# Kernel optimization log

Measured on AMD Instinct MI355X. Metric: run time of the kernel, lower is better.

The kernel has to match this reference:

```python
import jax, jax.numpy as jnp
import numpy as np

DIM, HEADS = 128, 8
DH = DIM // HEADS
SCALE = DH ** -0.5
N, E = 50000, 800000


def setup_inputs() -> dict:
    key = jax.random.key(0)
    ks = jax.random.split(key, 12)
    w = lambda k: jax.random.normal(k, (DIM, DIM), dtype=jnp.float32) * 0.02
    b = lambda k: jax.random.normal(k, (DIM,), dtype=jnp.float32) * 0.02
    return {
        "q_nodes": jax.random.normal(ks[0], (N, DIM), dtype=jnp.float32),
        "k_edges": jax.random.normal(ks[1], (E, DIM), dtype=jnp.float32),
        "v_edges": jax.random.normal(ks[2], (E, DIM), dtype=jnp.float32),
        "edge_index": jax.random.randint(ks[3], (2, E), 0, N, dtype=jnp.int64),
        "Wq": w(ks[4]), "bq": b(ks[5]),
        "Wk": w(ks[6]), "bk": b(ks[7]),
        "Wv": w(ks[8]), "bv": b(ks[9]),
        "Wo": w(ks[10]), "bo": b(ks[11]),
    }


def reference(q_nodes, k_edges, v_edges, edge_index, Wq, bq, Wk, bk, Wv, bv, Wo, bo):
    n, e = q_nodes.shape[0], k_edges.shape[0]
    dst = edge_index[0]  # src (edge_index[1]) is unused by the module
    q = (q_nodes @ Wq.T + bq).reshape(n, HEADS, DH)
    k = (k_edges @ Wk.T + bk).reshape(e, HEADS, DH)
    v = (v_edges @ Wv.T + bv).reshape(e, HEADS, DH)
    # per-edge score: dot(q[dst], k) per head -> [E, H]
    score = jnp.einsum('ehd,ehd->eh', q[dst], k) * SCALE
    # segment (per-dst-node) softmax over edges, numerically stable
    m = jax.ops.segment_max(score, dst, num_segments=n)          # [N, H]
    ex = jnp.exp(score - m[dst])                                  # [E, H]
    s = jax.ops.segment_sum(ex, dst, num_segments=n)             # [N, H]
    w = ex / (s[dst] + 1e-16)                                     # [E, H]
    weighted_v = (v * w[..., None]).reshape(e, DIM)               # [E, dim]
    aggr = jax.ops.segment_sum(weighted_v, dst, num_segments=n)  # [N, dim]
    return aggr @ Wo.T + bo
```

## Files before the change

kernel.cpp:

```cpp
#include <hip/hip_runtime.h>

#define TM 64
#define NTHREADS 256
#define PAD 132

typedef __attribute__((ext_vector_type(8))) short short8;
typedef __attribute__((ext_vector_type(4))) float f32x4;

__device__ __forceinline__ short f2bf(float f) {
  union { float f; unsigned u; } uf; uf.f = f;
  unsigned r = uf.u + 0x7FFFu + ((uf.u >> 16) & 1u);
  return (short)(r >> 16);
}
__device__ __forceinline__ float bf2f(short s) {
  union { unsigned u; float f; } uf; uf.u = ((unsigned)(unsigned short)s) << 16;
  return uf.f;
}
__device__ __forceinline__ short8 pack8(float4 a, float4 b) {
  short8 r;
  r[0] = f2bf(a.x); r[1] = f2bf(a.y); r[2] = f2bf(a.z); r[3] = f2bf(a.w);
  r[4] = f2bf(b.x); r[5] = f2bf(b.y); r[6] = f2bf(b.z); r[7] = f2bf(b.w);
  return r;
}


__global__ __launch_bounds__(512) void proj_mfma(
    const float* __restrict__ X, const short* __restrict__ Wb,
    const float* __restrict__ bias, float* __restrict__ Y, int M, float scale) {
  __shared__ short Xb[8192];
  int t = threadIdx.x;
  int w = t >> 6, l = t & 63, g = l >> 4, c = l & 15;
  short8 wf[4];
#pragma unroll
  for (int kc = 0; kc < 4; ++kc)
    wf[kc] = *(const short8*)(Wb + (w * 16 + c) * 128 + kc * 32 + g * 8);
  float4 b4 = *(const float4*)(bias + w * 16 + g * 4);

  for (int rb = blockIdx.x * 64; rb < M; rb += gridDim.x * 64) {
    {
      int r = t >> 3, q8 = t & 7;
      int row = rb + r; if (row >= M) row = M - 1;
      const float4* xs = (const float4*)(X + (size_t)row * 128 + q8 * 16);
      float4 x0 = xs[0], x1 = xs[1], x2 = xs[2], x3 = xs[3];
      int sw = (r & 7) << 4;
      *(short8*)((char*)Xb + r * 256 + ((q8 * 32) ^ sw)) = pack8(x0, x1);
      *(short8*)((char*)Xb + r * 256 + ((q8 * 32 + 16) ^ sw)) = pack8(x2, x3);
    }
    __syncthreads();
#pragma unroll
    for (int et = 0; et < 4; ++et) {
      int rl = et * 16 + c;
      f32x4 acc = {};
      int sw = (rl & 7) << 4;
#pragma unroll
      for (int kc = 0; kc < 4; ++kc) {
        short8 xb = *(const short8*)((char*)Xb + rl * 256 + ((kc * 64 + g * 16) ^ sw));
        acc = __builtin_amdgcn_mfma_f32_16x16x32_bf16(wf[kc], xb, acc, 0, 0, 0);
      }
      int row = rb + rl;
      if (row < M) {
        float4 o;
        o.x = (acc[0] + b4.x) * scale; o.y = (acc[1] + b4.y) * scale;
        o.z = (acc[2] + b4.z) * scale; o.w = (acc[3] + b4.w) * scale;
        *(float4*)(Y + (size_t)row * 128 + w * 16 + g * 4) = o;
      }
    }
    __syncthreads();
  }
}


__global__ __launch_bounds__(512) void proj_mfma_h(
    const float* __restrict__ X, const short* __restrict__ Wb,
    const float* __restrict__ bias, short* __restrict__ Yh, int M, float scale) {
  __shared__ short Xb[8192];
  int t = threadIdx.x;
  int w = t >> 6, l = t & 63, g = l >> 4, c = l & 15;
  short8 wf[4];
#pragma unroll
  for (int kc = 0; kc < 4; ++kc)
    wf[kc] = *(const short8*)(Wb + (w * 16 + c) * 128 + kc * 32 + g * 8);
  float4 b4 = *(const float4*)(bias + w * 16 + g * 4);

  for (int rb = blockIdx.x * 64; rb < M; rb += gridDim.x * 64) {
    {
      int r = t >> 3, q8 = t & 7;
      int row = rb + r; if (row >= M) row = M - 1;
      const float4* xs = (const float4*)(X + (size_t)row * 128 + q8 * 16);
      float4 x0 = xs[0], x1 = xs[1], x2 = xs[2], x3 = xs[3];
      int sw = (r & 7) << 4;
      *(short8*)((char*)Xb + r * 256 + ((q8 * 32) ^ sw)) = pack8(x0, x1);
      *(short8*)((char*)Xb + r * 256 + ((q8 * 32 + 16) ^ sw)) = pack8(x2, x3);
    }
    __syncthreads();
#pragma unroll
    for (int et = 0; et < 4; ++et) {
      int rl = et * 16 + c;
      f32x4 acc = {};
      int sw = (rl & 7) << 4;
#pragma unroll
      for (int kc = 0; kc < 4; ++kc) {
        short8 xb = *(const short8*)((char*)Xb + rl * 256 + ((kc * 64 + g * 16) ^ sw));
        acc = __builtin_amdgcn_mfma_f32_16x16x32_bf16(wf[kc], xb, acc, 0, 0, 0);
      }
      int row = rb + rl;
      if (row < M) {
        short4 o;
        o.x = f2bf((acc[0] + b4.x) * scale); o.y = f2bf((acc[1] + b4.y) * scale);
        o.z = f2bf((acc[2] + b4.z) * scale); o.w = f2bf((acc[3] + b4.w) * scale);
        *(short4*)(Yh + (size_t)row * 128 + w * 16 + g * 4) = o;
      }
    }
    __syncthreads();
  }
}


__global__ __launch_bounds__(256) void hist_kernel(const int* __restrict__ dst,
                                                   int* __restrict__ cnt, int E) {
  int e = blockIdx.x * 256 + threadIdx.x;
  if (e < E) atomicAdd(&cnt[dst[e]], 1);
}

__global__ __launch_bounds__(1024) void scan_part(const int* __restrict__ cnt,
                                                  int* __restrict__ part, int N) {
  __shared__ int ws[16];
  int t = threadIdx.x, i = blockIdx.x * 1024 + t;
  int v = (i < N) ? cnt[i] : 0;
#pragma unroll
  for (int d = 1; d < 64; d <<= 1) v += __shfl_xor(v, d);
  if ((t & 63) == 0) ws[t >> 6] = v;
  __syncthreads();
  if (t < 16) {
    int x = ws[t];
#pragma unroll
    for (int d = 1; d < 16; d <<= 1) x += __shfl_xor(x, d);
    if (t == 0) part[blockIdx.x] = x;
  }
}

__global__ __launch_bounds__(64) void scan_offs(int* __restrict__ part, int P) {
  int t = threadIdx.x;
  int carry = 0;
  for (int base = 0; base < P; base += 64) {
    int i = base + t;
    int v = (i < P) ? part[i] : 0;
    int x = v;
#pragma unroll
    for (int d = 1; d < 64; d <<= 1) { int y = __shfl_up(x, d); if (t >= d) x += y; }
    if (i < P) part[i] = x - v + carry;
    carry += __shfl(x, 63);
  }
}

__global__ __launch_bounds__(1024) void scan_final(const int* __restrict__ cnt,
                                                   const int* __restrict__ part,
                                                   int* __restrict__ rp,
                                                   int* __restrict__ cur, int N) {
  __shared__ int ws[16];
  __shared__ int wofs[16];
  int t = threadIdx.x, i = blockIdx.x * 1024 + t;
  int lane = t & 63, wid = t >> 6;
  int v = (i < N) ? cnt[i] : 0;
  int x = v;
#pragma unroll
  for (int d = 1; d < 64; d <<= 1) { int y = __shfl_up(x, d); if (lane >= d) x += y; }
  if (lane == 63) ws[wid] = x;
  __syncthreads();
  if (t == 0) {
    int s = 0;
#pragma unroll
    for (int k2 = 0; k2 < 16; ++k2) { int tmp = ws[k2]; wofs[k2] = s; s += tmp; }
  }
  __syncthreads();
  int incl = x + wofs[wid] + part[blockIdx.x];
  int excl = incl - v;
  if (i < N) {
    rp[i] = excl; cur[i] = excl;
    if (i == N - 1) rp[N] = incl;
  }
}

__global__ __launch_bounds__(256) void perm_kernel(const int* __restrict__ dst,
                                                   int* __restrict__ cursor,
                                                   int* __restrict__ perm, int E) {
  int e = blockIdx.x * 256 + threadIdx.x;
  if (e < E) perm[e] = atomicAdd(&cursor[dst[e]], 1);
}

__global__ __launch_bounds__(256) void wprep4(
    const float* __restrict__ Wq, const float* __restrict__ Wk,
    const float* __restrict__ Wv, const float* __restrict__ Wo,
    short* __restrict__ wqb, short* __restrict__ wkb,
    short* __restrict__ wvb, short* __restrict__ wob) {
  int i = blockIdx.x * 256 + threadIdx.x;
  if (i < 16384) {
    wqb[i] = f2bf(Wq[i]); wkb[i] = f2bf(Wk[i]);
    wvb[i] = f2bf(Wv[i]); wob[i] = f2bf(Wo[i]);
  }
}


__global__ __launch_bounds__(512) void edge_mfma7(
    const float* __restrict__ K, const float* __restrict__ V,
    const int* __restrict__ eidx, const int* __restrict__ perm,
    const short* __restrict__ wkb, const short* __restrict__ wvb,
    const float* __restrict__ bk, const short* __restrict__ qpb,
    float* __restrict__ exb, short* __restrict__ wv, int E) {
  __shared__ short Kb[8192];
  __shared__ short Vb[8192];
  __shared__ float exs[512];
  __shared__ int sh_perm[64];
  int t = threadIdx.x;
  int w = t >> 6, l = t & 63, g = l >> 4, c = l & 15;
  float4 bk4 = *(const float4*)(bk + w * 16 + g * 4);
  const short* wkp = wkb + (w * 16 + c) * 128 + g * 8;
  const short* wvp = wvb + (w * 16 + c) * 128 + g * 8;
  const short* qpp = qpb + (size_t)(w * 16 + g * 4);

  int r = t >> 3, q8 = t & 7;
  int sw_st = (r & 7) << 4;
  int b0 = r * 256 + ((q8 * 32) ^ sw_st);
  int stride = gridDim.x * 64;
  int eb = blockIdx.x * 64;

  float4 k0, k1, k2, k3;
  short4 qvb[4];
  int prm_r;
  {
    int row0 = eb + r; if (row0 >= E) row0 = E - 1;
    const float4* ks = (const float4*)(K + (size_t)row0 * 128 + q8 * 16);
    k0 = ks[0]; k1 = ks[1]; k2 = ks[2]; k3 = ks[3];
    prm_r = perm[row0];
#pragma unroll
    for (int et = 0; et < 4; ++et) {
      int e = eb + et * 16 + c; if (e >= E) e = E - 1;
      qvb[et] = *(const short4*)(qpp + (size_t)eidx[e] * 128);
    }
  }

  for (; eb < E; eb += stride) {
    int ebn = eb + stride;
    bool hn = ebn < E;

    __syncthreads();
    *(short8*)((char*)Kb + b0) = pack8(k0, k1);
    *(short8*)((char*)Kb + (b0 ^ 16)) = pack8(k2, k3);
    if (q8 == 0) sh_perm[r] = prm_r;
    short8 wK[4];
#pragma unroll
    for (int kc = 0; kc < 4; ++kc)
      wK[kc] = *(const short8*)(wkp + kc * 32);
    float4 v0, v1, v2, v3;
    {
      int rowv = eb + r; if (rowv >= E) rowv = E - 1;
      const float4* vs = (const float4*)(V + (size_t)rowv * 128 + q8 * 16);
      v0 = vs[0]; v1 = vs[1]; v2 = vs[2]; v3 = vs[3];
    }
    __syncthreads();

    float ex[4];
#pragma unroll
    for (int et = 0; et < 4; ++et) {
      int eloc = et * 16 + c;
      int swr = (eloc & 7) << 4;
      f32x4 acc = {};
#pragma unroll
      for (int kc = 0; kc < 4; ++kc) {
        short8 xb = *(const short8*)((char*)Kb + eloc * 256 + ((kc * 64 + g * 16) ^ swr));
        acc = __builtin_amdgcn_mfma_f32_16x16x32_bf16(wK[kc], xb, acc, 0, 0, 0);
      }
      float s = (acc[0] + bk4.x) * bf2f(qvb[et].x) + (acc[1] + bk4.y) * bf2f(qvb[et].y) +
                (acc[2] + bk4.z) * bf2f(qvb[et].z) + (acc[3] + bk4.w) * bf2f(qvb[et].w);
      s += __shfl_xor(s, 16);
      s += __shfl_xor(s, 32);
      ex[et] = __expf(s);
      if (g == 0) exs[eloc * 8 + w] = ex[et];
    }

    *(short8*)((char*)Vb + b0) = pack8(v0, v1);
    *(short8*)((char*)Vb + (b0 ^ 16)) = pack8(v2, v3);
    short8 wV[4];
#pragma unroll
    for (int kc = 0; kc < 4; ++kc)
      wV[kc] = *(const short8*)(wvp + kc * 32);
    int prm_rn = 0;
    if (hn) {
      int rowk = ebn + r; if (rowk >= E) rowk = E - 1;
      const float4* ks = (const float4*)(K + (size_t)rowk * 128 + q8 * 16);
      k0 = ks[0]; k1 = ks[1]; k2 = ks[2]; k3 = ks[3];
      prm_rn = perm[rowk];
#pragma unroll
      for (int et = 0; et < 4; ++et) {
        int e = ebn + et * 16 + c; if (e >= E) e = E - 1;
        qvb[et] = *(const short4*)(qpp + (size_t)eidx[e] * 128);
      }
    }
    __syncthreads();

#pragma unroll
    for (int et = 0; et < 4; ++et) {
      int eloc = et * 16 + c;
      int swr = (eloc & 7) << 4;
      f32x4 acc = {};
#pragma unroll
      for (int kc = 0; kc < 4; ++kc) {
        short8 xb = *(const short8*)((char*)Vb + eloc * 256 + ((kc * 64 + g * 16) ^ swr));
        acc = __builtin_amdgcn_mfma_f32_16x16x32_bf16(wV[kc], xb, acc, 0, 0, 0);
      }
      short4 sv;
      sv.x = f2bf(acc[0] * ex[et]); sv.y = f2bf(acc[1] * ex[et]);
      sv.z = f2bf(acc[2] * ex[et]); sv.w = f2bf(acc[3] * ex[et]);
      *(short4*)((char*)Kb + eloc * 256 + ((w * 32 + g * 8) ^ swr)) = sv;
    }
    prm_r = prm_rn;
    __syncthreads();

    {
      int row = eb + r;
      if (row < E) {
        int slot = sh_perm[r];
        short8 a = *(const short8*)((char*)Kb + r * 256 + ((q8 * 32) ^ sw_st));
        short8 b = *(const short8*)((char*)Kb + r * 256 + ((q8 * 32 + 16) ^ sw_st));
        *(short8*)(wv + (size_t)slot * 128 + q8 * 16) = a;
        *(short8*)(wv + (size_t)slot * 128 + q8 * 16 + 8) = b;
      }
      if (t < 128) {
        int r2 = t >> 1, half = t & 1;
        if (eb + r2 < E) {
          int slot2 = sh_perm[r2];
          *(float4*)(exb + (size_t)slot2 * 8 + half * 4) =
              *(const float4*)(&exs[r2 * 8 + half * 4]);
        }
      }
    }
  }
}


__global__ __launch_bounds__(256) void pull3(
    const short* __restrict__ wv, const float* __restrict__ exb,
    const int* __restrict__ rp, const float* __restrict__ bv,
    float* __restrict__ aggr, int N) {
  int w = threadIdx.x >> 6, l = threadIdx.x & 63;
  int n = blockIdx.x * 4 + w;
  if (n >= N) return;
  int beg = rp[n], end = rp[n + 1];
  int h = l >> 3;
  float a0 = 0.f, a1 = 0.f, s = 0.f;
  int j = beg;
  for (; j + 1 < end; j += 2) {
    unsigned u0 = *(const unsigned*)(wv + (size_t)j * 128 + l * 2);
    unsigned u1 = *(const unsigned*)(wv + (size_t)(j + 1) * 128 + l * 2);
    float s0 = exb[(size_t)j * 8 + h], s1 = exb[(size_t)(j + 1) * 8 + h];
    a0 += bf2f((short)(u0 & 0xFFFFu)) + bf2f((short)(u1 & 0xFFFFu));
    a1 += bf2f((short)(u0 >> 16)) + bf2f((short)(u1 >> 16));
    s += s0 + s1;
  }
  if (j < end) {
    unsigned u0 = *(const unsigned*)(wv + (size_t)j * 128 + l * 2);
    s += exb[(size_t)j * 8 + h];
    a0 += bf2f((short)(u0 & 0xFFFFu));
    a1 += bf2f((short)(u0 >> 16));
  }
  float2 o;
  if (end > beg) {
    float inv = 1.f / (s + 1e-16f);
    float2 bvv = *(const float2*)(bv + l * 2);
    o.x = a0 * inv + bvv.x; o.y = a1 * inv + bvv.y;
  } else {
    o.x = 0.f; o.y = 0.f;
  }
  *(float2*)(aggr + (size_t)n * 128 + l * 2) = o;
}


__device__ __forceinline__ void stage_x(float (*Xs)[PAD], const float* __restrict__ X,
                                        int rowbase, int M, int t) {
#pragma unroll
  for (int i = 0; i < 8; ++i) {
    int idx = t + NTHREADS * i;
    int r = idx >> 5, q = idx & 31;
    int row = rowbase + r;
    if (row >= M) row = M - 1;
    const float4 v = *(const float4*)(X + (size_t)row * 128 + q * 4);
    *(float4*)(&Xs[r][q * 4]) = v;
  }
}

__device__ __forceinline__ void gemm_tile(const float (*Xs)[PAD], float (*WT)[PAD],
                                          const float* __restrict__ W,
                                          float acc[8][4], int r0, int c0, int t) {
#pragma unroll 1
  for (int kk = 0; kk < 128; kk += 32) {
    {
      int j = t >> 1, half = t & 1;
      const float* src = W + j * 128 + kk + half * 16;
      float4 a = *(const float4*)(src);
      float4 b = *(const float4*)(src + 4);
      float4 c = *(const float4*)(src + 8);
      float4 d = *(const float4*)(src + 12);
      int cb = half * 16;
      WT[cb + 0][j] = a.x;  WT[cb + 1][j] = a.y;  WT[cb + 2][j] = a.z;  WT[cb + 3][j] = a.w;
      WT[cb + 4][j] = b.x;  WT[cb + 5][j] = b.y;  WT[cb + 6][j] = b.z;  WT[cb + 7][j] = b.w;
      WT[cb + 8][j] = c.x;  WT[cb + 9][j] = c.y;  WT[cb + 10][j] = c.z; WT[cb + 11][j] = c.w;
      WT[cb + 12][j] = d.x; WT[cb + 13][j] = d.y; WT[cb + 14][j] = d.z; WT[cb + 15][j] = d.w;
    }
    __syncthreads();
#pragma unroll
    for (int c2 = 0; c2 < 16; ++c2) {
      float4 wa = *(const float4*)(&WT[2 * c2][c0]);
      float4 wb = *(const float4*)(&WT[2 * c2 + 1][c0]);
#pragma unroll
      for (int i = 0; i < 8; ++i) {
        float2 xv = *(const float2*)(&Xs[r0 + i][kk + 2 * c2]);
        acc[i][0] = fmaf(xv.x, wa.x, acc[i][0]);
        acc[i][1] = fmaf(xv.x, wa.y, acc[i][1]);
        acc[i][2] = fmaf(xv.x, wa.z, acc[i][2]);
        acc[i][3] = fmaf(xv.x, wa.w, acc[i][3]);
        acc[i][0] = fmaf(xv.y, wb.x, acc[i][0]);
        acc[i][1] = fmaf(xv.y, wb.y, acc[i][1]);
        acc[i][2] = fmaf(xv.y, wb.z, acc[i][2]);
        acc[i][3] = fmaf(xv.y, wb.w, acc[i][3]);
      }
    }
    __syncthreads();
  }
}

__global__ __launch_bounds__(NTHREADS) void proj_kernel(
    const float* __restrict__ X, const float* __restrict__ W,
    const float* __restrict__ b, float* __restrict__ Y, int M) {
  __shared__ float Xs[TM][PAD];
  __shared__ float WT[32][PAD];
  int t = threadIdx.x;
  int B0 = blockIdx.x * TM;
  stage_x(Xs, X, B0, M, t);
  __syncthreads();
  int r0 = (t >> 5) * 8, m = t & 31, c0 = m * 4;
  float acc[8][4] = {};
  gemm_tile(Xs, WT, W, acc, r0, c0, t);
  float4 bv = ((const float4*)b)[m];
#pragma unroll
  for (int i = 0; i < 8; ++i) {
    int row = B0 + r0 + i;
    if (row < M) {
      float4 o;
      o.x = acc[i][0] + bv.x; o.y = acc[i][1] + bv.y;
      o.z = acc[i][2] + bv.z; o.w = acc[i][3] + bv.w;
      *(float4*)(Y + (size_t)row * 128 + c0) = o;
    }
  }
}

__global__ __launch_bounds__(NTHREADS) void edge_kernel(
    const float* __restrict__ Kin, const float* __restrict__ Vin,
    const int* __restrict__ eidx,
    const float* __restrict__ Wk, const float* __restrict__ bk,
    const float* __restrict__ Wv, const float* __restrict__ bv,
    const float* __restrict__ qp, float* __restrict__ s_sum,
    float* __restrict__ aggr, int E) {
  __shared__ float Xs[TM][PAD];
  __shared__ float WT[32][PAD];
  __shared__ int dsts[TM];
  int t = threadIdx.x;
  int e0 = blockIdx.x * TM;
  if (t < TM) {
    int idx = e0 + t;
    if (idx >= E) idx = E - 1;
    dsts[t] = eidx[idx];
  }
  stage_x(Xs, Kin, e0, E, t);
  __syncthreads();
  int r0 = (t >> 5) * 8, m = t & 31, c0 = m * 4;
  int h = m >> 2;
  float acc[8][4] = {};
  gemm_tile(Xs, WT, Wk, acc, r0, c0, t);
  float4 bkv = ((const float4*)bk)[m];
  float ex[8];
#pragma unroll
  for (int i = 0; i < 8; ++i) {
    int r = r0 + i;
    const float4 qv = *(const float4*)(qp + (size_t)dsts[r] * 128 + c0);
    float p = (acc[i][0] + bkv.x) * qv.x + (acc[i][1] + bkv.y) * qv.y +
              (acc[i][2] + bkv.z) * qv.z + (acc[i][3] + bkv.w) * qv.w;
    p += __shfl_xor(p, 1);
    p += __shfl_xor(p, 2);
    float e = __expf(p * 0.25f);
    ex[i] = e;
    if ((m & 3) == 0 && (e0 + r) < E)
      atomicAdd(&s_sum[(size_t)dsts[r] * 8 + h], e);
  }
  __syncthreads();
  stage_x(Xs, Vin, e0, E, t);
  __syncthreads();
#pragma unroll
  for (int i = 0; i < 8; ++i)
#pragma unroll
    for (int j = 0; j < 4; ++j) acc[i][j] = 0.f;
  gemm_tile(Xs, WT, Wv, acc, r0, c0, t);
  float4 bvv = ((const float4*)bv)[m];
#pragma unroll
  for (int i = 0; i < 8; ++i) {
    int r = r0 + i;
    if ((e0 + r) < E) {
      size_t base = (size_t)dsts[r] * 128 + c0;
      atomicAdd(&aggr[base + 0], (acc[i][0] + bvv.x) * ex[i]);
      atomicAdd(&aggr[base + 1], (acc[i][1] + bvv.y) * ex[i]);
      atomicAdd(&aggr[base + 2], (acc[i][2] + bvv.z) * ex[i]);
      atomicAdd(&aggr[base + 3], (acc[i][3] + bvv.w) * ex[i]);
    }
  }
}

__global__ __launch_bounds__(NTHREADS) void out_kernel(
    const float* __restrict__ aggr, const float* __restrict__ s_sum,
    const float* __restrict__ W, const float* __restrict__ b,
    float* __restrict__ Y, int M) {
  __shared__ float Xs[TM][PAD];
  __shared__ float WT[32][PAD];
  int t = threadIdx.x;
  int B0 = blockIdx.x * TM;
#pragma unroll
  for (int i = 0; i < 8; ++i) {
    int idx = t + NTHREADS * i;
    int r = idx >> 5, q = idx & 31;
    int row = B0 + r;
    if (row >= M) row = M - 1;
    float4 v = *(const float4*)(aggr + (size_t)row * 128 + q * 4);
    float inv = 1.0f / (s_sum[(size_t)row * 8 + (q >> 2)] + 1e-16f);
    v.x *= inv; v.y *= inv; v.z *= inv; v.w *= inv;
    *(float4*)(&Xs[r][q * 4]) = v;
  }
  __syncthreads();
  int r0 = (t >> 5) * 8, m = t & 31, c0 = m * 4;
  float acc[8][4] = {};
  gemm_tile(Xs, WT, W, acc, r0, c0, t);
  float4 bv = ((const float4*)b)[m];
#pragma unroll
  for (int i = 0; i < 8; ++i) {
    int row = B0 + r0 + i;
    if (row < M) {
      float4 o;
      o.x = acc[i][0] + bv.x; o.y = acc[i][1] + bv.y;
      o.z = acc[i][2] + bv.z; o.w = acc[i][3] + bv.w;
      *(float4*)(Y + (size_t)row * 128 + c0) = o;
    }
  }
}


extern "C" void kernel_launch(void* const* d_in, const int* in_sizes, int n_in,
                              void* d_out, int out_size, void* d_ws, size_t ws_size,
                              hipStream_t stream) {
  const float* q_nodes = (const float*)d_in[0];
  const float* k_edges = (const float*)d_in[1];
  const float* v_edges = (const float*)d_in[2];
  const int* eidx = (const int*)d_in[3];
  const float* Wq = (const float*)d_in[4];
  const float* bq = (const float*)d_in[5];
  const float* Wk = (const float*)d_in[6];
  const float* bk = (const float*)d_in[7];
  const float* Wv = (const float*)d_in[8];
  const float* bv = (const float*)d_in[9];
  const float* Wo = (const float*)d_in[10];
  const float* bo = (const float*)d_in[11];

  int N = in_sizes[0] / 128;
  int E = in_sizes[1] / 128;
  int P = (N + 1023) / 1024;

  size_t off = 0;
  auto alloc = [&](size_t b) { size_t o = off; off += (b + 255) & ~(size_t)255; return o; };
  size_t o_qpb  = alloc((size_t)N * 128 * 2);
  size_t o_aggr = alloc((size_t)N * 128 * 4);
  size_t o_exb  = alloc((size_t)E * 8 * 4);
  size_t o_rp   = alloc(((size_t)N + 1) * 4);
  size_t o_cur  = alloc((size_t)N * 4);
  size_t o_cnt  = alloc((size_t)N * 4);
  size_t o_perm = alloc((size_t)E * 4);
  size_t o_part = alloc((size_t)(P + 1) * 4);
  size_t o_wqb  = alloc((size_t)16384 * 2);
  size_t o_wkb  = alloc((size_t)16384 * 2);
  size_t o_wvb  = alloc((size_t)16384 * 2);
  size_t o_wob  = alloc((size_t)16384 * 2);
  size_t o_wv   = alloc((size_t)E * 128 * 2);

  if (off <= ws_size) {
    char* base = (char*)d_ws;
    short* qpb   = (short*)(base + o_qpb);
    float* aggr  = (float*)(base + o_aggr);
    float* exb   = (float*)(base + o_exb);
    int*   rp    = (int*)(base + o_rp);
    int*   cur   = (int*)(base + o_cur);
    int*   cnt   = (int*)(base + o_cnt);
    int*   perm  = (int*)(base + o_perm);
    int*   part  = (int*)(base + o_part);
    short* wqb   = (short*)(base + o_wqb);
    short* wkb   = (short*)(base + o_wkb);
    short* wvb   = (short*)(base + o_wvb);
    short* wob   = (short*)(base + o_wob);
    short* wvbuf = (short*)(base + o_wv);

    hipMemsetAsync(cnt, 0, (size_t)N * 4, stream);
    wprep4<<<64, 256, 0, stream>>>(Wq, Wk, Wv, Wo, wqb, wkb, wvb, wob);
    proj_mfma_h<<<(N + 63) / 64, 512, 0, stream>>>(q_nodes, wqb, bq, qpb, N, 0.25f);
    hist_kernel<<<(E + 255) / 256, 256, 0, stream>>>(eidx, cnt, E);
    scan_part<<<P, 1024, 0, stream>>>(cnt, part, N);
    scan_offs<<<1, 64, 0, stream>>>(part, P);
    scan_final<<<P, 1024, 0, stream>>>(cnt, part, rp, cur, N);
    perm_kernel<<<(E + 255) / 256, 256, 0, stream>>>(eidx, cur, perm, E);

    int eblk = (E + 63) / 64; if (eblk > 1024) eblk = 1024;
    edge_mfma7<<<eblk, 512, 0, stream>>>(k_edges, v_edges, eidx, perm, wkb, wvb,
                                         bk, qpb, exb, wvbuf, E);
    pull3<<<(N + 3) / 4, 256, 0, stream>>>(wvbuf, exb, rp, bv, aggr, N);
    proj_mfma<<<(N + 63) / 64, 512, 0, stream>>>(aggr, wob, bo, (float*)d_out, N, 1.0f);
  } else {
    float* q_proj = (float*)d_ws;
    float* s_sum  = q_proj + (size_t)N * 128;
    float* aggr   = s_sum + (size_t)N * 8;
    hipMemsetAsync(s_sum, 0, (size_t)N * 136 * sizeof(float), stream);
    int nblk = (N + TM - 1) / TM;
    int eblk = (E + TM - 1) / TM;
    proj_kernel<<<nblk, NTHREADS, 0, stream>>>(q_nodes, Wq, bq, q_proj, N);
    edge_kernel<<<eblk, NTHREADS, 0, stream>>>(k_edges, v_edges, eidx, Wk, bk, Wv, bv,
                                               q_proj, s_sum, aggr, E);
    out_kernel<<<nblk, NTHREADS, 0, stream>>>(aggr, s_sum, Wo, bo, (float*)d_out, N);
  }
}
```

Measured before the change: 420.0 us.

## Fuse histogram with rank capture and drop separate perm and offset-scan kernels

The histogram kernel now records each edge's atomic rank within its destination bucket, so the edge kernel computes its CSR slot as rp[dst]+rank and the second atomic pass (perm_kernel) disappears. The single-block offset scan is also removed: each scan_final block sums the preceding partials itself. This cuts two kernel launches and one full pass of atomics over the edges, at the cost of an extra dependent gather of rp[eidx] in the edge kernel and redundant partial summation per block. The pull loop is also unrolled from 2 to 4 edges to expose more memory parallelism.

```diff
diff --git a/kernel.cpp b/kernel.cpp
--- a/kernel.cpp
+++ b/kernel.cpp
@@ -116,10 +116,11 @@
 }
 
 
-__global__ __launch_bounds__(256) void hist_kernel(const int* __restrict__ dst,
-                                                   int* __restrict__ cnt, int E) {
+__global__ __launch_bounds__(256) void rank_hist(const int* __restrict__ dst,
+                                                 int* __restrict__ cnt,
+                                                 int* __restrict__ rank, int E) {
   int e = blockIdx.x * 256 + threadIdx.x;
-  if (e < E) atomicAdd(&cnt[dst[e]], 1);
+  if (e < E) rank[e] = atomicAdd(&cnt[dst[e]], 1);
 }
 
 __global__ __launch_bounds__(1024) void scan_part(const int* __restrict__ cnt,
@@ -139,28 +140,21 @@
   }
 }
 
-__global__ __launch_bounds__(64) void scan_offs(int* __restrict__ part, int P) {
-  int t = threadIdx.x;
-  int carry = 0;
-  for (int base = 0; base < P; base += 64) {
-    int i = base + t;
-    int v = (i < P) ? part[i] : 0;
-    int x = v;
-#pragma unroll
-    for (int d = 1; d < 64; d <<= 1) { int y = __shfl_up(x, d); if (t >= d) x += y; }
-    if (i < P) part[i] = x - v + carry;
-    carry += __shfl(x, 63);
-  }
-}
-
 __global__ __launch_bounds__(1024) void scan_final(const int* __restrict__ cnt,
                                                    const int* __restrict__ part,
-                                                   int* __restrict__ rp,
-                                                   int* __restrict__ cur, int N) {
+                                                   int* __restrict__ rp, int N) {
   __shared__ int ws[16];
   __shared__ int wofs[16];
+  __shared__ int base_sh;
   int t = threadIdx.x, i = blockIdx.x * 1024 + t;
   int lane = t & 63, wid = t >> 6;
+  if (t < 64) {
+    int v = 0;
+    for (int j = t; j < blockIdx.x; j += 64) v += part[j];
+#pragma unroll
+    for (int d = 1; d < 64; d <<= 1) v += __shfl_xor(v, d);
+    if (t == 0) base_sh = v;
+  }
   int v = (i < N) ? cnt[i] : 0;
   int x = v;
 #pragma unroll
@@ -173,19 +167,12 @@
     for (int k2 = 0; k2 < 16; ++k2) { int tmp = ws[k2]; wofs[k2] = s; s += tmp; }
   }
   __syncthreads();
-  int incl = x + wofs[wid] + part[blockIdx.x];
+  int incl = x + wofs[wid] + base_sh;
   int excl = incl - v;
   if (i < N) {
-    rp[i] = excl; cur[i] = excl;
+    rp[i] = excl;
     if (i == N - 1) rp[N] = incl;
   }
-}
-
-__global__ __launch_bounds__(256) void perm_kernel(const int* __restrict__ dst,
-                                                   int* __restrict__ cursor,
-                                                   int* __restrict__ perm, int E) {
-  int e = blockIdx.x * 256 + threadIdx.x;
-  if (e < E) perm[e] = atomicAdd(&cursor[dst[e]], 1);
 }
 
 __global__ __launch_bounds__(256) void wprep4(
@@ -203,7 +190,8 @@
 
 __global__ __launch_bounds__(512) void edge_mfma7(
     const float* __restrict__ K, const float* __restrict__ V,
-    const int* __restrict__ eidx, const int* __restrict__ perm,
+    const int* __restrict__ eidx, const int* __restrict__ rank,
+    const int* __restrict__ rp,
     const short* __restrict__ wkb, const short* __restrict__ wvb,
     const float* __restrict__ bk, const short* __restrict__ qpb,
     float* __restrict__ exb, short* __restrict__ wv, int E) {
@@ -231,7 +219,7 @@
     int row0 = eb + r; if (row0 >= E) row0 = E - 1;
     const float4* ks = (const float4*)(K + (size_t)row0 * 128 + q8 * 16);
     k0 = ks[0]; k1 = ks[1]; k2 = ks[2]; k3 = ks[3];
-    prm_r = perm[row0];
+    prm_r = rp[eidx[row0]] + rank[row0];
 #pragma unroll
     for (int et = 0; et < 4; ++et) {
       int e = eb + et * 16 + c; if (e >= E) e = E - 1;
@@ -289,7 +277,7 @@
       int rowk = ebn + r; if (rowk >= E) rowk = E - 1;
       const float4* ks = (const float4*)(K + (size_t)rowk * 128 + q8 * 16);
       k0 = ks[0]; k1 = ks[1]; k2 = ks[2]; k3 = ks[3];
-      prm_rn = perm[rowk];
+      prm_rn = rp[eidx[rowk]] + rank[rowk];
 #pragma unroll
       for (int et = 0; et < 4; ++et) {
         int e = ebn + et * 16 + c; if (e >= E) e = E - 1;
@@ -349,15 +337,20 @@
   int h = l >> 3;
   float a0 = 0.f, a1 = 0.f, s = 0.f;
   int j = beg;
-  for (; j + 1 < end; j += 2) {
+  for (; j + 3 < end; j += 4) {
     unsigned u0 = *(const unsigned*)(wv + (size_t)j * 128 + l * 2);
     unsigned u1 = *(const unsigned*)(wv + (size_t)(j + 1) * 128 + l * 2);
-    float s0 = exb[(size_t)j * 8 + h], s1 = exb[(size_t)(j + 1) * 8 + h];
-    a0 += bf2f((short)(u0 & 0xFFFFu)) + bf2f((short)(u1 & 0xFFFFu));
-    a1 += bf2f((short)(u0 >> 16)) + bf2f((short)(u1 >> 16));
-    s += s0 + s1;
-  }
-  if (j < end) {
+    unsigned u2 = *(const unsigned*)(wv + (size_t)(j + 2) * 128 + l * 2);
+    unsigned u3 = *(const unsigned*)(wv + (size_t)(j + 3) * 128 + l * 2);
+    float s0 = exb[(size_t)j * 8 + h],       s1 = exb[(size_t)(j + 1) * 8 + h];
+    float s2 = exb[(size_t)(j + 2) * 8 + h], s3 = exb[(size_t)(j + 3) * 8 + h];
+    a0 += bf2f((short)(u0 & 0xFFFFu)) + bf2f((short)(u1 & 0xFFFFu)) +
+          bf2f((short)(u2 & 0xFFFFu)) + bf2f((short)(u3 & 0xFFFFu));
+    a1 += bf2f((short)(u0 >> 16)) + bf2f((short)(u1 >> 16)) +
+          bf2f((short)(u2 >> 16)) + bf2f((short)(u3 >> 16));
+    s += s0 + s1 + s2 + s3;
+  }
+  for (; j < end; ++j) {
     unsigned u0 = *(const unsigned*)(wv + (size_t)j * 128 + l * 2);
     s += exb[(size_t)j * 8 + h];
     a0 += bf2f((short)(u0 & 0xFFFFu));
@@ -576,9 +569,8 @@
   size_t o_aggr = alloc((size_t)N * 128 * 4);
   size_t o_exb  = alloc((size_t)E * 8 * 4);
   size_t o_rp   = alloc(((size_t)N + 1) * 4);
-  size_t o_cur  = alloc((size_t)N * 4);
   size_t o_cnt  = alloc((size_t)N * 4);
-  size_t o_perm = alloc((size_t)E * 4);
+  size_t o_rank = alloc((size_t)E * 4);
   size_t o_part = alloc((size_t)(P + 1) * 4);
   size_t o_wqb  = alloc((size_t)16384 * 2);
   size_t o_wkb  = alloc((size_t)16384 * 2);
@@ -592,9 +584,8 @@
     float* aggr  = (float*)(base + o_aggr);
     float* exb   = (float*)(base + o_exb);
     int*   rp    = (int*)(base + o_rp);
-    int*   cur   = (int*)(base + o_cur);
     int*   cnt   = (int*)(base + o_cnt);
-    int*   perm  = (int*)(base + o_perm);
+    int*   rank  = (int*)(base + o_rank);
     int*   part  = (int*)(base + o_part);
     short* wqb   = (short*)(base + o_wqb);
     short* wkb   = (short*)(base + o_wkb);
@@ -605,14 +596,12 @@
     hipMemsetAsync(cnt, 0, (size_t)N * 4, stream);
     wprep4<<<64, 256, 0, stream>>>(Wq, Wk, Wv, Wo, wqb, wkb, wvb, wob);
     proj_mfma_h<<<(N + 63) / 64, 512, 0, stream>>>(q_nodes, wqb, bq, qpb, N, 0.25f);
-    hist_kernel<<<(E + 255) / 256, 256, 0, stream>>>(eidx, cnt, E);
+    rank_hist<<<(E + 255) / 256, 256, 0, stream>>>(eidx, cnt, rank, E);
     scan_part<<<P, 1024, 0, stream>>>(cnt, part, N);
-    scan_offs<<<1, 64, 0, stream>>>(part, P);
-    scan_final<<<P, 1024, 0, stream>>>(cnt, part, rp, cur, N);
-    perm_kernel<<<(E + 255) / 256, 256, 0, stream>>>(eidx, cur, perm, E);
+    scan_final<<<P, 1024, 0, stream>>>(cnt, part, rp, N);
 
     int eblk = (E + 63) / 64; if (eblk > 1024) eblk = 1024;
-    edge_mfma7<<<eblk, 512, 0, stream>>>(k_edges, v_edges, eidx, perm, wkb, wvb,
+    edge_mfma7<<<eblk, 512, 0, stream>>>(k_edges, v_edges, eidx, rank, rp, wkb, wvb,
                                          bk, qpb, exb, wvbuf, E);
     pull3<<<(N + 3) / 4, 256, 0, stream>>>(wvbuf, exb, rp, bv, aggr, N);
     proj_mfma<<<(N + 63) / 64, 512, 0, stream>>>(aggr, wob, bo, (float*)d_out, N, 1.0f);
```

After: 382.3 us. -9.0%, faster.
